# Performance work log

Hardware: AMD Instinct MI355X
Metric: run time of the kernel (lower is better)

## Reference

```python
import jax, jax.numpy as jnp
import numpy as np

N = 8192
DIN = 128
DOUT = 128
EPS = 1e-7
GAMMA_MAX = 1e7


def _mobius_scalar_mul(r, x):
    # Moebius scalar multiplication on the Poincare ball (c=1):
    # r (.) x = tanh(r * arctanh(||x||)) * x / ||x||
    n = jnp.linalg.norm(x, axis=-1, keepdims=True)
    n_safe = jnp.clip(n, EPS, 1.0 - EPS)
    return jnp.tanh(r * jnp.arctanh(n_safe)) * x / n_safe


def _logmap0(x):
    n = jnp.linalg.norm(x, axis=-1, keepdims=True)
    n_safe = jnp.clip(n, EPS, 1.0 - EPS)
    return jnp.arctanh(n_safe) * x / n_safe


def _expmap0(v):
    n = jnp.linalg.norm(v, axis=-1, keepdims=True)
    n_safe = jnp.maximum(n, EPS)
    return jnp.tanh(n_safe) * v / n_safe


def setup_inputs() -> dict:
    key = jax.random.key(0)
    k1, k2, k3, k4 = jax.random.split(key, 4)
    # node features inside the Poincare ball (small norm)
    x = 0.01 * jax.random.normal(k1, (N, DIN), dtype=jnp.float32)
    # sparse-ish binary adjacency stored dense (module treats adj as dense [N,N])
    adj = (jax.random.uniform(k2, (N, N)) < 0.004).astype(jnp.float32)
    W = 0.05 * jax.random.normal(k3, (DIN, DOUT), dtype=jnp.float32)
    b = 0.05 * jax.random.normal(k4, (DOUT,), dtype=jnp.float32)
    return {"x": x, "adj": adj, "W": W, "b": b}


def reference(x, adj, W, b):
    n = adj.shape[0]
    # adj <- I + adj, then symmetric degree normalization D^{-1/2} A D^{-1/2}
    a = jnp.eye(n, dtype=adj.dtype) + adj
    D = 1.0 / jnp.sqrt(jnp.sum(a, axis=1))
    a = a * D[:, None] * D[None, :]
    # gyromidpoint-style weighted aggregation (gamma broadcast over rows, as in torch)
    r2 = jnp.sum(x * x, axis=-1, keepdims=True)            # [N,1]
    gamma = jnp.minimum(2.0 / (1.0 - r2), GAMMA_MAX)        # [N,1]
    num = a * gamma                                          # [N,N]
    den = jnp.sum(a * (gamma - 1.0), axis=-1, keepdims=True)  # [N,1]
    coef = num / den                                         # [N,N]
    aggr = coef @ x                                          # [N,DIN]
    aggr = _mobius_scalar_mul(0.5, aggr)
    # PoincareFC: logmap0 -> linear -> act -> expmap0 (to_tan=False)
    u = _logmap0(aggr)
    y = jax.nn.relu(u @ W + b)
    return _expmap0(y)
```

## Files before the change

### kernel.cpp

```cpp
#include <hip/hip_runtime.h>
#include <cstdint>
#include <cstddef>

#define N_NODES 8192
#define DIN 128
#define CAP 128
#define EPSF 1e-7f

typedef unsigned short u16;
typedef unsigned int u32;

__global__ __launch_bounds__(256) void k_build(const float4* __restrict__ adj,
                                               u16* __restrict__ cols,
                                               int* __restrict__ counts,
                                               float* __restrict__ Dv) {
    const int lane = threadIdx.x & 63;
    const int row  = blockIdx.x * 4 + (threadIdx.x >> 6);
    const float4* rp = adj + (size_t)row * (N_NODES / 4);
    u16* cl = cols + (size_t)row * CAP;
    const unsigned long long lt_mask = (1ULL << lane) - 1ULL;
    const int s = row & 31;

    int base = 0;
#pragma unroll 8
    for (int ii = 0; ii < N_NODES / 256; ++ii) {
        const int it = (ii + s) & 31;
        float4 v = rp[it * 64 + lane];
        int cb = it * 256 + lane * 4;
        {
            bool nz = (v.x != 0.0f);
            unsigned long long m = __ballot(nz);
            if (nz) { int p = base + __popcll(m & lt_mask); if (p < CAP) cl[p] = (u16)(cb + 0); }
            base += __popcll(m);
        }
        {
            bool nz = (v.y != 0.0f);
            unsigned long long m = __ballot(nz);
            if (nz) { int p = base + __popcll(m & lt_mask); if (p < CAP) cl[p] = (u16)(cb + 1); }
            base += __popcll(m);
        }
        {
            bool nz = (v.z != 0.0f);
            unsigned long long m = __ballot(nz);
            if (nz) { int p = base + __popcll(m & lt_mask); if (p < CAP) cl[p] = (u16)(cb + 2); }
            base += __popcll(m);
        }
        {
            bool nz = (v.w != 0.0f);
            unsigned long long m = __ballot(nz);
            if (nz) { int p = base + __popcll(m & lt_mask); if (p < CAP) cl[p] = (u16)(cb + 3); }
            base += __popcll(m);
        }
    }
    if (lane == 0) {
        counts[row] = base;
        Dv[row] = 1.0f / sqrtf(1.0f + (float)base);
    }
}

__device__ __forceinline__ float waveSum(float v) {
#pragma unroll
    for (int m = 32; m >= 1; m >>= 1) v += __shfl_xor(v, m, 64);
    return v;
}

__global__ __launch_bounds__(256) void k_fused(const float* __restrict__ x,
                                               const float* __restrict__ Dv,
                                               const u16* __restrict__ cols,
                                               const int* __restrict__ counts,
                                               const float* __restrict__ W,
                                               const float* __restrict__ b,
                                               float* __restrict__ out) {
    __shared__ u16   colsL[4][CAP];
    __shared__ float djL[4][CAP];
    __shared__ float uL[4][DIN];
    __shared__ float red[8];

    const int tid = threadIdx.x;
    const int w   = tid >> 6;
    const int l   = tid & 63;
    const int row0 = blockIdx.x * 4;
    const int row  = row0 + w;
    const float2* x2 = (const float2*)x;

    int c = counts[row];
    if (c > CAP) c = CAP;

    ((u32*)colsL[w])[l] = ((const u32*)(cols + (size_t)row * CAP))[l];
    {
        int k0 = 2 * l, k1 = 2 * l + 1;
        int j0 = colsL[w][k0], j1 = colsL[w][k1];
        djL[w][k0] = (k0 < c) ? Dv[j0] : 0.0f;
        djL[w][k1] = (k1 < c) ? Dv[j1] : 0.0f;
    }
    const float2 xi = x2[(size_t)row * 64 + l];
    const float  Di = Dv[row];

    float ax = Di * xi.x, ay = Di * xi.y;
    float sumw = Di;
#pragma unroll 4
    for (int k = 0; k < c; ++k) {
        int   j  = colsL[w][k];
        float dj = djL[w][k];
        sumw += dj;
        float2 xj = x2[(size_t)j * 64 + l];
        ax = fmaf(dj, xj.x, ax);
        ay = fmaf(dj, xj.y, ay);
    }

    float r2 = waveSum(fmaf(xi.x, xi.x, xi.y * xi.y));
    float gamma = fminf(2.0f / (1.0f - r2), 1e7f);
    float sg = gamma / ((gamma - 1.0f) * sumw);
    ax *= sg; ay *= sg;

    float n2 = waveSum(fmaf(ax, ax, ay * ay));
    float n  = sqrtf(n2);
    float nsafe = fminf(fmaxf(n, EPSF), 1.0f - EPSF);
    float t  = tanhf(0.5f * atanhf(nsafe));
    float nm = t * (n / nsafe);
    float nmsafe = fminf(fmaxf(nm, EPSF), 1.0f - EPSF);
    float us = (atanhf(nmsafe) / nmsafe) * (t / nsafe);
    ((float2*)uL[w])[l] = make_float2(us * ax, us * ay);

    __syncthreads();

    const int h = tid >> 7;
    const int d = tid & 127;
    const float bd = b[d];
    float a0 = bd, a1 = bd;
    const float* Wc = W + d;
    const float* u0 = uL[2 * h];
    const float* u1 = uL[2 * h + 1];
#pragma unroll 8
    for (int k = 0; k < DIN; ++k) {
        float wkd = Wc[(size_t)k * DIN];
        a0 = fmaf(u0[k], wkd, a0);
        a1 = fmaf(u1[k], wkd, a1);
    }

    float y0 = fmaxf(a0, 0.0f), y1 = fmaxf(a1, 0.0f);
    float s0 = waveSum(y0 * y0);
    float s1 = waveSum(y1 * y1);
    if (l == 0) { red[w * 2] = s0; red[w * 2 + 1] = s1; }
    __syncthreads();
    float ss0 = red[4 * h + 0] + red[4 * h + 2];
    float ss1 = red[4 * h + 1] + red[4 * h + 3];
    float ns0 = fmaxf(sqrtf(ss0), EPSF);
    float ns1 = fmaxf(sqrtf(ss1), EPSF);
    float sc0 = tanhf(ns0) / ns0;
    float sc1 = tanhf(ns1) / ns1;
    out[(size_t)(row0 + 2 * h) * DIN + d]     = y0 * sc0;
    out[(size_t)(row0 + 2 * h + 1) * DIN + d] = y1 * sc1;
}

extern "C" void kernel_launch(void* const* d_in, const int* in_sizes, int n_in,
                              void* d_out, int out_size, void* d_ws, size_t ws_size,
                              hipStream_t stream) {
    const float* x   = (const float*)d_in[0];
    const float* adj = (const float*)d_in[1];
    const float* W   = (const float*)d_in[2];
    const float* b   = (const float*)d_in[3];
    float* out = (float*)d_out;

    char* ws = (char*)d_ws;
    int*   counts = (int*)ws;
    float* Dv     = (float*)(ws + 32768);
    u16*   cols   = (u16*)(ws + 65536);

    hipLaunchKernelGGL(k_build, dim3(N_NODES / 4), dim3(256), 0, stream,
                       (const float4*)adj, cols, counts, Dv);
    hipLaunchKernelGGL(k_fused, dim3(N_NODES / 4), dim3(256), 0, stream,
                       x, Dv, cols, counts, W, b, out);
}
```

Baseline: 396.1 us.

## Rewrite adjacency compaction with nontemporal loads, OR-based skip and LDS atomic slots

The build kernel now reads two 16-byte chunks per lane with nontemporal loads and ORs the raw bits to skip all-zero chunks under a wave ballot. Instead of four ballot/popcount steps per element, each lane with nonzeros counts them by summing the floats (valid only for 0/1 values) and reserves a slot through an LDS atomic. This cuts per-element ALU and ballot work on the streaming pass over the 256MB adjacency. In exchange, column order within a row is no longer sorted, and the count assumes binary adjacency entries. The fused kernel also guards its column-index reads so it no longer looks up Dv with garbage indices.

```diff
diff --git a/kernel.cpp b/kernel.cpp
--- a/kernel.cpp
+++ b/kernel.cpp
@@ -9,52 +9,50 @@
 
 typedef unsigned short u16;
 typedef unsigned int u32;
+typedef u32 nuint4 __attribute__((ext_vector_type(4)));
 
-__global__ __launch_bounds__(256) void k_build(const float4* __restrict__ adj,
+__global__ __launch_bounds__(256) void k_build(const nuint4* __restrict__ adj,
                                                u16* __restrict__ cols,
                                                int* __restrict__ counts,
                                                float* __restrict__ Dv) {
+    __shared__ int cnt[4];
     const int lane = threadIdx.x & 63;
-    const int row  = blockIdx.x * 4 + (threadIdx.x >> 6);
-    const float4* rp = adj + (size_t)row * (N_NODES / 4);
+    const int w    = threadIdx.x >> 6;
+    const int row  = blockIdx.x * 4 + w;
+    if (lane == 0) cnt[w] = 0;
+    const nuint4* rp = adj + (size_t)row * (N_NODES / 4);
     u16* cl = cols + (size_t)row * CAP;
-    const unsigned long long lt_mask = (1ULL << lane) - 1ULL;
-    const int s = row & 31;
 
-    int base = 0;
-#pragma unroll 8
-    for (int ii = 0; ii < N_NODES / 256; ++ii) {
-        const int it = (ii + s) & 31;
-        float4 v = rp[it * 64 + lane];
-        int cb = it * 256 + lane * 4;
-        {
-            bool nz = (v.x != 0.0f);
-            unsigned long long m = __ballot(nz);
-            if (nz) { int p = base + __popcll(m & lt_mask); if (p < CAP) cl[p] = (u16)(cb + 0); }
-            base += __popcll(m);
-        }
-        {
-            bool nz = (v.y != 0.0f);
-            unsigned long long m = __ballot(nz);
-            if (nz) { int p = base + __popcll(m & lt_mask); if (p < CAP) cl[p] = (u16)(cb + 1); }
-            base += __popcll(m);
-        }
-        {
-            bool nz = (v.z != 0.0f);
-            unsigned long long m = __ballot(nz);
-            if (nz) { int p = base + __popcll(m & lt_mask); if (p < CAP) cl[p] = (u16)(cb + 2); }
-            base += __popcll(m);
-        }
-        {
-            bool nz = (v.w != 0.0f);
-            unsigned long long m = __ballot(nz);
-            if (nz) { int p = base + __popcll(m & lt_mask); if (p < CAP) cl[p] = (u16)(cb + 3); }
-            base += __popcll(m);
+#pragma unroll 2
+    for (int it = 0; it < 16; ++it) {
+        nuint4 a = __builtin_nontemporal_load(&rp[it * 128 + lane]);
+        nuint4 b = __builtin_nontemporal_load(&rp[it * 128 + 64 + lane]);
+        u32 oa = (a.x | a.y) | (a.z | a.w);
+        u32 ob = (b.x | b.y) | (b.z | b.w);
+        if (__ballot((oa | ob) != 0)) {
+            if ((oa | ob) != 0) {
+                float cf = ((__uint_as_float(a.x) + __uint_as_float(a.y)) +
+                            (__uint_as_float(a.z) + __uint_as_float(a.w))) +
+                           ((__uint_as_float(b.x) + __uint_as_float(b.y)) +
+                            (__uint_as_float(b.z) + __uint_as_float(b.w)));
+                int c = (int)cf;
+                int p = atomicAdd(&cnt[w], c);
+                int ca = it * 512 + 4 * lane;
+                int cb = ca + 256;
+                u32 ws8[8] = {a.x, a.y, a.z, a.w, b.x, b.y, b.z, b.w};
+#pragma unroll
+                for (int k = 0; k < 8; ++k)
+                    if (ws8[k]) {
+                        if (p < CAP) cl[p] = (u16)((k < 4 ? ca : cb - 4) + k);
+                        ++p;
+                    }
+            }
         }
     }
+    int deg = cnt[w];
     if (lane == 0) {
-        counts[row] = base;
-        Dv[row] = 1.0f / sqrtf(1.0f + (float)base);
+        counts[row] = deg;
+        Dv[row] = 1.0f / sqrtf(1.0f + (float)deg);
     }
 }
 
@@ -89,7 +87,8 @@
     ((u32*)colsL[w])[l] = ((const u32*)(cols + (size_t)row * CAP))[l];
     {
         int k0 = 2 * l, k1 = 2 * l + 1;
-        int j0 = colsL[w][k0], j1 = colsL[w][k1];
+        int j0 = (k0 < c) ? colsL[w][k0] : 0;
+        int j1 = (k1 < c) ? colsL[w][k1] : 0;
         djL[w][k0] = (k0 < c) ? Dv[j0] : 0.0f;
         djL[w][k1] = (k1 < c) ? Dv[j1] : 0.0f;
     }
@@ -168,7 +167,7 @@
     u16*   cols   = (u16*)(ws + 65536);
 
     hipLaunchKernelGGL(k_build, dim3(N_NODES / 4), dim3(256), 0, stream,
-                       (const float4*)adj, cols, counts, Dv);
+                       (const nuint4*)adj, cols, counts, Dv);
     hipLaunchKernelGGL(k_fused, dim3(N_NODES / 4), dim3(256), 0, stream,
                        x, Dv, cols, counts, W, b, out);
 }
```

Measured after the change: 367.9 us. -7.1%, faster.
